# Optimization experiments

Hardware: AMD Instinct MI355X
Metric: run time of the kernel (lower is better)

The kernel has to match this reference:

```python
import jax, jax.numpy as jnp
import numpy as np

N_STATE = 1024
N_HEAD = 16
HEAD_DIM = N_STATE // N_HEAD
SEQLENS = [1024, 896, 768, 640, 512, 384, 896, 1024]  # sum = 6144
TOTAL = sum(SEQLENS)


def setup_inputs() -> dict:
    key = jax.random.key(0)
    ks = jax.random.split(key, 8)
    s = 0.02
    cu = jnp.asarray(np.concatenate([[0], np.cumsum(SEQLENS)]), dtype=jnp.int32)
    return {
        "x": jax.random.normal(ks[0], (TOTAL, N_STATE), jnp.float32),
        "cu_seqlens": cu,
        "Wq": jax.random.normal(ks[1], (N_STATE, N_STATE), jnp.float32) * s,
        "bq": jax.random.normal(ks[2], (N_STATE,), jnp.float32) * s,
        "Wk": jax.random.normal(ks[3], (N_STATE, N_STATE), jnp.float32) * s,
        "Wv": jax.random.normal(ks[4], (N_STATE, N_STATE), jnp.float32) * s,
        "bv": jax.random.normal(ks[5], (N_STATE,), jnp.float32) * s,
        "Wo": jax.random.normal(ks[6], (N_STATE, N_STATE), jnp.float32) * s,
        "bo": jax.random.normal(ks[7], (N_STATE,), jnp.float32) * s,
    }


def reference(x, cu_seqlens, Wq, bq, Wk, Wv, bv, Wo, bo):
    # cu_seqlens is a static (host) quantity in the original (used via .tolist())
    cu = np.asarray(jax.device_get(cu_seqlens))
    seqlens = cu[1:] - cu[:-1]
    B = len(seqlens)
    Lmax = int(seqlens.max())

    q = x @ Wq.T + bq              # [T, n_state]
    k = x @ Wk.T                   # key has no bias
    v = x @ Wv.T + bv

    # static pad/unpad index maps (honoring the ragged structure)
    ar = np.arange(Lmax)
    valid = ar[None, :] < seqlens[:, None]             # [B, Lmax]
    idx = np.where(valid, cu[:-1, None] + ar[None, :], 0)
    unpad_idx = np.nonzero(valid.reshape(-1))[0]       # flat positions of real tokens
    valid_j = jnp.asarray(valid)

    def pad(t):  # [T, n_state] -> [B, Lmax, H, D], zeros in padding
        p = jnp.where(valid_j[:, :, None], t[idx], 0.0)
        return p.reshape(B, Lmax, N_HEAD, HEAD_DIM)

    qp, kp, vp = pad(q), pad(k), pad(v)
    scale = HEAD_DIM ** -0.5
    # torch adds the bool mask (True->1.0) after masked_fill(mask==0, -max):
    # valid keys get +1.0 (softmax-invariant shift), invalid keys get -finfo.max
    big_neg = jnp.finfo(x.dtype).max
    add_mask = jnp.where(valid_j, 1.0, -big_neg)[:, None, None, :]  # [B,1,1,Lmax]

    scores = jnp.einsum("bqhd,bkhd->bhqk", qp, kp) * scale + add_mask
    weights = jax.nn.softmax(scores, axis=-1)
    ctx = jnp.einsum("bhqk,bkhd->bqhd", weights, vp)   # [B, Lmax, H, D]
    ctx_flat = ctx.reshape(B * Lmax, N_STATE)[unpad_idx]  # [T, n_state]
    return ctx_flat @ Wo.T + bo
```

## Files before the change

### kernel.cpp

```cpp
#include <hip/hip_runtime.h>

typedef unsigned short u16;
typedef unsigned int u32;
typedef __attribute__((ext_vector_type(8))) short bf16x8;
typedef __attribute__((ext_vector_type(4))) float f32x4;

#define MFMA_BF16(a, b, c) __builtin_amdgcn_mfma_f32_16x16x32_bf16((a), (b), (c), 0, 0, 0)

#define QSCALE 0.18033688011112042f

__device__ __forceinline__ u16 f2bf(float f) {
    union { float f; unsigned u; } v; v.f = f;
    return (u16)((v.u + 0x7FFFu + ((v.u >> 16) & 1u)) >> 16);
}

__device__ __forceinline__ u32 pkbf(float a, float b) {
    union { float f; unsigned u; } x, y; x.f = a; y.f = b;
    return ((x.u + 0x8000u) >> 16) | ((y.u + 0x8000u) & 0xFFFF0000u);
}

__device__ __forceinline__ void async16(const void* g, void* l) {
    __builtin_amdgcn_global_load_lds(
        (const __attribute__((address_space(1))) void*)g,
        (__attribute__((address_space(3))) void*)l, 16, 0, 0);
}

__global__ __launch_bounds__(256) void cvt_all(
    const float* __restrict__ x, const float* __restrict__ Wq, const float* __restrict__ Wk,
    const float* __restrict__ Wv, const float* __restrict__ Wo,
    u16* __restrict__ xb, u16* __restrict__ Wqb, u16* __restrict__ Wkb,
    u16* __restrict__ Wvb, u16* __restrict__ Wob) {
    int b = blockIdx.x;
    const float* src; u16* dst; int base;
    if (b < 6144)      { src = x;  dst = xb;  base = b; }
    else if (b < 7168) { src = Wq; dst = Wqb; base = b - 6144; }
    else if (b < 8192) { src = Wk; dst = Wkb; base = b - 7168; }
    else if (b < 9216) { src = Wv; dst = Wvb; base = b - 8192; }
    else               { src = Wo; dst = Wob; base = b - 9216; }
    int i = base * 256 + threadIdx.x;
    float4 v = ((const float4*)src)[i];
    unsigned long long pk = (unsigned long long)f2bf(v.x)
                          | ((unsigned long long)f2bf(v.y) << 16)
                          | ((unsigned long long)f2bf(v.z) << 32)
                          | ((unsigned long long)f2bf(v.w) << 48);
    *(unsigned long long*)(dst + (size_t)i * 4) = pk;
}

__global__ __launch_bounds__(256) void gemm_qkv(
    const u16* __restrict__ xb,
    const u16* __restrict__ Wqb, const u16* __restrict__ Wkb, const u16* __restrict__ Wvb,
    const float* __restrict__ bq, const float* __restrict__ bv,
    u16* __restrict__ qb, u16* __restrict__ kb, u16* __restrict__ vbT) {
    __shared__ __align__(16) u16 As[128 * 64];
    __shared__ __align__(16) u16 Bs[128 * 64];
    const int tid = threadIdx.x;
    const int m0 = blockIdx.x << 7;
    const int by = blockIdx.y;
    const int buf = by >> 3;
    const int n0 = (by & 7) << 7;
    const u16* __restrict__ W = (buf == 0) ? Wqb : (buf == 1) ? Wkb : Wvb;

    const int rr = tid >> 3;
    const int cg = tid & 7;
    const int wv = tid >> 6, lane = tid & 63, g = lane >> 4, c = lane & 15;
    const int wm = (wv & 1) << 6, wn = (wv >> 1) << 6;

    const int sw = (cg ^ (rr & 7)) << 3;
    const u16* gA[4]; const u16* gB[4];
#pragma unroll
    for (int r = 0; r < 4; ++r) {
        gA[r] = xb + (size_t)(m0 + (r << 5) + rr) * 1024 + sw;
        gB[r] = W + (size_t)(n0 + (r << 5) + rr) * 1024 + sw;
    }

    f32x4 zero = {0.f, 0.f, 0.f, 0.f};
    f32x4 acc[4][4];
#pragma unroll
    for (int i = 0; i < 4; ++i)
#pragma unroll
        for (int j = 0; j < 4; ++j) acc[i][j] = zero;

    if (buf < 2) {
        for (int kt = 0; kt < 16; ++kt) {
            const int k0 = kt << 6;
            __syncthreads();
#pragma unroll
            for (int r = 0; r < 4; ++r) {
                async16(gA[r] + k0, &As[(r << 11) + tid * 8]);
                async16(gB[r] + k0, &Bs[(r << 11) + tid * 8]);
            }
            __syncthreads();
#pragma unroll
            for (int ks = 0; ks < 2; ++ks) {
                bf16x8 af[4], bb[4];
#pragma unroll
                for (int i = 0; i < 4; ++i) {
                    int ra = wm + (i << 4) + c;
                    af[i] = *(const bf16x8*)(&As[ra * 64 + ((((ks << 2) + g) ^ (ra & 7)) << 3)]);
                    int rb = wn + (i << 4) + c;
                    bb[i] = *(const bf16x8*)(&Bs[rb * 64 + ((((ks << 2) + g) ^ (rb & 7)) << 3)]);
                }
#pragma unroll
                for (int i = 0; i < 4; ++i)
#pragma unroll
                    for (int j = 0; j < 4; ++j) acc[i][j] = MFMA_BF16(bb[j], af[i], acc[i][j]);
            }
        }
    } else {
        for (int kt = 0; kt < 16; ++kt) {
            const int k0 = kt << 6;
            __syncthreads();
#pragma unroll
            for (int r = 0; r < 4; ++r) {
                async16(gA[r] + k0, &As[(r << 11) + tid * 8]);
                async16(gB[r] + k0, &Bs[(r << 11) + tid * 8]);
            }
            __syncthreads();
#pragma unroll
            for (int ks = 0; ks < 2; ++ks) {
                bf16x8 af[4], bb[4];
#pragma unroll
                for (int i = 0; i < 4; ++i) {
                    int ra = wm + (i << 4) + c;
                    af[i] = *(const bf16x8*)(&As[ra * 64 + ((((ks << 2) + g) ^ (ra & 7)) << 3)]);
                    int rb = wn + (i << 4) + c;
                    bb[i] = *(const bf16x8*)(&Bs[rb * 64 + ((((ks << 2) + g) ^ (rb & 7)) << 3)]);
                }
#pragma unroll
                for (int i = 0; i < 4; ++i)
#pragma unroll
                    for (int j = 0; j < 4; ++j) acc[i][j] = MFMA_BF16(af[i], bb[j], acc[i][j]);
            }
        }
    }

    if (buf == 0) {
#pragma unroll
        for (int j = 0; j < 4; ++j) {
            int ncol = n0 + wn + (j << 4) + (g << 2);
            const float4 b4 = *(const float4*)(bq + ncol);
#pragma unroll
            for (int i = 0; i < 4; ++i) {
                const size_t mrow = (size_t)(m0 + wm + (i << 4) + c) * 1024;
                unsigned long long pk =
                      (unsigned long long)f2bf((acc[i][j][0] + b4.x) * QSCALE)
                    | ((unsigned long long)f2bf((acc[i][j][1] + b4.y) * QSCALE) << 16)
                    | ((unsigned long long)f2bf((acc[i][j][2] + b4.z) * QSCALE) << 32)
                    | ((unsigned long long)f2bf((acc[i][j][3] + b4.w) * QSCALE) << 48);
                *(unsigned long long*)(qb + mrow + ncol) = pk;
            }
        }
    } else if (buf == 1) {
#pragma unroll
        for (int j = 0; j < 4; ++j) {
            int ncol = n0 + wn + (j << 4) + (g << 2);
#pragma unroll
            for (int i = 0; i < 4; ++i) {
                const size_t mrow = (size_t)(m0 + wm + (i << 4) + c) * 1024;
                unsigned long long pk =
                      (unsigned long long)f2bf(acc[i][j][0])
                    | ((unsigned long long)f2bf(acc[i][j][1]) << 16)
                    | ((unsigned long long)f2bf(acc[i][j][2]) << 32)
                    | ((unsigned long long)f2bf(acc[i][j][3]) << 48);
                *(unsigned long long*)(kb + mrow + ncol) = pk;
            }
        }
    } else {
#pragma unroll
        for (int j = 0; j < 4; ++j) {
            int col = n0 + wn + (j << 4) + c;
            float bias = bv[col];
#pragma unroll
            for (int i = 0; i < 4; ++i) {
                int trow = m0 + wm + (i << 4) + (g << 2);
                unsigned long long pk =
                      (unsigned long long)f2bf(acc[i][j][0] + bias)
                    | ((unsigned long long)f2bf(acc[i][j][1] + bias) << 16)
                    | ((unsigned long long)f2bf(acc[i][j][2] + bias) << 32)
                    | ((unsigned long long)f2bf(acc[i][j][3] + bias) << 48);
                *(unsigned long long*)(vbT + (size_t)col * 6144 + trow) = pk;
            }
        }
    }
}

__global__ __launch_bounds__(256) void gemm_out(
    const u16* __restrict__ ctxb, const u16* __restrict__ Wob,
    const float* __restrict__ bo, float* __restrict__ out) {
    __shared__ __align__(16) u16 As[64 * 64];
    __shared__ __align__(16) u16 Bs[64 * 64];
    const int tid = threadIdx.x;
    const int m0 = blockIdx.x << 6;
    const int n0 = blockIdx.y << 6;
    const int rr = tid >> 3, cg = tid & 7;
    const int wv = tid >> 6, lane = tid & 63, g = lane >> 4, c = lane & 15;
    const int wm = (wv & 1) << 5, wn = (wv >> 1) << 5;

    const int sw = (cg ^ (rr & 7)) << 3;
    const u16* gA[2]; const u16* gB[2];
#pragma unroll
    for (int r = 0; r < 2; ++r) {
        gA[r] = ctxb + (size_t)(m0 + (r << 5) + rr) * 1024 + sw;
        gB[r] = Wob + (size_t)(n0 + (r << 5) + rr) * 1024 + sw;
    }

    f32x4 zero = {0.f, 0.f, 0.f, 0.f};
    f32x4 acc[2][2];
#pragma unroll
    for (int i = 0; i < 2; ++i)
#pragma unroll
        for (int j = 0; j < 2; ++j) acc[i][j] = zero;

    for (int kt = 0; kt < 16; ++kt) {
        const int k0 = kt << 6;
        __syncthreads();
#pragma unroll
        for (int r = 0; r < 2; ++r) {
            async16(gA[r] + k0, &As[(r << 11) + tid * 8]);
            async16(gB[r] + k0, &Bs[(r << 11) + tid * 8]);
        }
        __syncthreads();
#pragma unroll
        for (int ks = 0; ks < 2; ++ks) {
            bf16x8 af[2], bb[2];
#pragma unroll
            for (int i = 0; i < 2; ++i) {
                int ra = wm + (i << 4) + c;
                af[i] = *(const bf16x8*)(&As[ra * 64 + ((((ks << 2) + g) ^ (ra & 7)) << 3)]);
                int rb = wn + (i << 4) + c;
                bb[i] = *(const bf16x8*)(&Bs[rb * 64 + ((((ks << 2) + g) ^ (rb & 7)) << 3)]);
            }
#pragma unroll
            for (int i = 0; i < 2; ++i)
#pragma unroll
                for (int j = 0; j < 2; ++j) acc[i][j] = MFMA_BF16(bb[j], af[i], acc[i][j]);
        }
    }

#pragma unroll
    for (int i = 0; i < 2; ++i) {
        const size_t mrow = (size_t)(m0 + wm + (i << 4) + c) * 1024;
#pragma unroll
        for (int j = 0; j < 2; ++j) {
            int ncol = n0 + wn + (j << 4) + (g << 2);
            const float4 b4 = *(const float4*)(bo + ncol);
            float4 o;
            o.x = acc[i][j][0] + b4.x;
            o.y = acc[i][j][1] + b4.y;
            o.z = acc[i][j][2] + b4.z;
            o.w = acc[i][j][3] + b4.w;
            *(float4*)(out + mrow + ncol) = o;
        }
    }
}

__global__ __launch_bounds__(256) void attn_kernel(const u16* __restrict__ qb,
                                                   const u16* __restrict__ kb,
                                                   const u16* __restrict__ vbT,
                                                   u16* __restrict__ ctxb) {
    __shared__ __align__(16) u16 Ks[128 * 64];
    __shared__ __align__(16) u16 Vs[64 * 128];
    __shared__ __align__(16) u16 Ps[4 * 2048];

    const int tid = threadIdx.x;
    const int fid = blockIdx.x;
    const int xcd = fid & 7;
    const int slot = fid >> 3;
    const int h = (xcd << 1) + (slot >= 96 ? 1 : 0);
    const int q0 = (slot % 96) << 6;

    const int cuv[9] = {0, 1024, 1920, 2688, 3328, 3840, 4224, 5120, 6144};
    int s0 = 0, e0 = 6144;
#pragma unroll
    for (int i = 1; i < 8; ++i) {
        if (q0 >= cuv[i]) s0 = cuv[i];
        if (q0 < cuv[i] && cuv[i] < e0) e0 = cuv[i];
    }
    const int ntiles = (e0 - s0) >> 7;

    const int wv = tid >> 6, lane = tid & 63, g = lane >> 4, c = lane & 15;
    const int wrow = wv << 4;

    {
        const int rr = tid >> 3, cg = tid & 7;
#pragma unroll
        for (int r = 0; r < 2; ++r) {
            int row = (r << 5) + rr;
            async16(qb + (size_t)(q0 + row) * 1024 + (h << 6) + ((cg ^ (row & 7)) << 3),
                    Ps + (r << 11) + tid * 8);
        }
    }
    __syncthreads();

    bf16x8 qf[2];
#pragma unroll
    for (int ks = 0; ks < 2; ++ks) {
        int row = wrow + c;
        qf[ks] = *(const bf16x8*)(Ps + row * 64 + ((((ks << 2) + g) ^ (row & 7)) << 3));
    }

    float m_run = -1e30f, l_run = 0.f;
    f32x4 zero = {0.f, 0.f, 0.f, 0.f};
    f32x4 oacc[4];
#pragma unroll
    for (int nt = 0; nt < 4; ++nt) oacc[nt] = zero;

    const int pbase = (wv << 11) + c * 128;
    const int c7 = c & 7;

    for (int kt = 0; kt < ntiles; ++kt) {
        const int kv0 = s0 + (kt << 7);
        __syncthreads();
        {
            const int rr = tid >> 3, cg = tid & 7;
#pragma unroll
            for (int r = 0; r < 4; ++r) {
                int row = (r << 5) + rr;
                async16(kb + (size_t)(kv0 + row) * 1024 + (h << 6) + ((cg ^ (row & 7)) << 3),
                        Ks + (r << 11) + tid * 8);
            }
            const int rr2 = tid >> 4, cg2 = tid & 15;
#pragma unroll
            for (int r = 0; r < 4; ++r) {
                int row = (r << 4) + rr2;
                async16(vbT + (size_t)((h << 6) + row) * 6144 + kv0 + ((cg2 ^ (row & 15)) << 3),
                        Vs + (r << 11) + tid * 8);
            }
        }
        __syncthreads();

        f32x4 st[8];
#pragma unroll
        for (int mt = 0; mt < 8; ++mt) st[mt] = zero;
#pragma unroll
        for (int mt = 0; mt < 8; ++mt) {
            int row = (mt << 4) + c;
            int sw = row & 7;
#pragma unroll
            for (int ks = 0; ks < 2; ++ks) {
                bf16x8 kf = *(const bf16x8*)(&Ks[row * 64 + ((((ks << 2) + g) ^ sw) << 3)]);
                st[mt] = MFMA_BF16(kf, qf[ks], st[mt]);
            }
        }

        float mx = st[0][0];
#pragma unroll
        for (int mt = 0; mt < 8; ++mt)
#pragma unroll
            for (int r = 0; r < 4; ++r) mx = fmaxf(mx, st[mt][r]);
        mx = fmaxf(mx, __shfl_xor(mx, 16, 64));
        mx = fmaxf(mx, __shfl_xor(mx, 32, 64));
        float mnew = fmaxf(m_run, mx);
        float alpha = exp2f(m_run - mnew);
        m_run = mnew;

        float rsum = 0.f;
#pragma unroll
        for (int mt = 0; mt < 8; ++mt) {
            float p0 = exp2f(st[mt][0] - mnew);
            float p1 = exp2f(st[mt][1] - mnew);
            float p2 = exp2f(st[mt][2] - mnew);
            float p3 = exp2f(st[mt][3] - mnew);
            rsum += (p0 + p1) + (p2 + p3);
            int ph = ((mt << 2) + g) ^ (c7 << 1);
            *(uint2*)(Ps + pbase + (ph << 2)) = make_uint2(pkbf(p0, p1), pkbf(p2, p3));
        }
        rsum += __shfl_xor(rsum, 16, 64);
        rsum += __shfl_xor(rsum, 32, 64);
        l_run = l_run * alpha + rsum;

        float al[4];
#pragma unroll
        for (int r = 0; r < 4; ++r) al[r] = __shfl(alpha, (g << 2) + r, 16);
#pragma unroll
        for (int nt = 0; nt < 4; ++nt)
#pragma unroll
            for (int r = 0; r < 4; ++r) oacc[nt][r] *= al[r];

#pragma unroll
        for (int ks = 0; ks < 4; ++ks) {
            int pg = ((ks << 2) + g) ^ c7;
            bf16x8 pf = *(const bf16x8*)(Ps + pbase + (pg << 3));
#pragma unroll
            for (int nt = 0; nt < 4; ++nt) {
                int vrow = (nt << 4) + c;
                bf16x8 vf = *(const bf16x8*)(&Vs[vrow * 128 + ((((ks << 2) + g) ^ (vrow & 15)) << 3)]);
                oacc[nt] = MFMA_BF16(pf, vf, oacc[nt]);
            }
        }
    }

    float inv = 1.0f / l_run;
    float invr[4];
#pragma unroll
    for (int r = 0; r < 4; ++r) invr[r] = __shfl(inv, (g << 2) + r, 16);
#pragma unroll
    for (int r = 0; r < 4; ++r) {
        size_t rowoff = (size_t)(q0 + wrow + (g << 2) + r) * 1024 + (h << 6);
#pragma unroll
        for (int nt = 0; nt < 4; ++nt)
            ctxb[rowoff + (nt << 4) + c] = f2bf(oacc[nt][r] * invr[r]);
    }
}

extern "C" void kernel_launch(void* const* d_in, const int* in_sizes, int n_in,
                              void* d_out, int out_size, void* d_ws, size_t ws_size,
                              hipStream_t stream) {
    const float* x  = (const float*)d_in[0];
    const float* Wq = (const float*)d_in[2];
    const float* bq = (const float*)d_in[3];
    const float* Wk = (const float*)d_in[4];
    const float* Wv = (const float*)d_in[5];
    const float* bv = (const float*)d_in[6];
    const float* Wo = (const float*)d_in[7];
    const float* bo = (const float*)d_in[8];
    float* out = (float*)d_out;

    u16* ws = (u16*)d_ws;
    u16* xb   = ws;
    u16* Wqb  = xb + 6291456;
    u16* Wkb  = Wqb + 1048576;
    u16* Wvb  = Wkb + 1048576;
    u16* Wob  = Wvb + 1048576;
    u16* qb   = Wob + 1048576;
    u16* kb   = qb + 6291456;
    u16* vbT  = kb + 6291456;
    u16* ctxb = xb;

    cvt_all<<<10240, 256, 0, stream>>>(x, Wq, Wk, Wv, Wo, xb, Wqb, Wkb, Wvb, Wob);
    gemm_qkv<<<dim3(48, 24), 256, 0, stream>>>(xb, Wqb, Wkb, Wvb, bq, bv, qb, kb, vbT);
    attn_kernel<<<1536, 256, 0, stream>>>(qb, kb, vbT, ctxb);
    gemm_out<<<dim3(96, 16), 256, 0, stream>>>(ctxb, Wob, bo, out);
}
```

Measured before the change: 236.9 us.

## Process 128 query rows per attention block to reuse K/V tiles

Each attention block now handles 128 queries (two 16-row sub-tiles per wave) instead of 64, halving the grid to 768 blocks so every K/V tile loaded into LDS is reused across twice as many queries. The first K/V tile is prefetched together with Q before the loop, which removes one barrier pair per block. The XCD-aware head/query mapping is dropped in favour of a plain h = fid/48 mapping. In exchange, register pressure goes up (two sets of output accumulators and running statistics), there are fewer blocks to spread across CUs, and L2 locality per XCD may change.

```diff
diff --git a/kernel.cpp b/kernel.cpp
--- a/kernel.cpp
+++ b/kernel.cpp
@@ -264,10 +264,8 @@
 
     const int tid = threadIdx.x;
     const int fid = blockIdx.x;
-    const int xcd = fid & 7;
-    const int slot = fid >> 3;
-    const int h = (xcd << 1) + (slot >= 96 ? 1 : 0);
-    const int q0 = (slot % 96) << 6;
+    const int h = fid / 48;
+    const int q0 = (fid % 48) << 7;
 
     const int cuv[9] = {0, 1024, 1920, 2688, 3328, 3840, 4224, 5120, 6144};
     int s0 = 0, e0 = 6144;
@@ -279,127 +277,147 @@
     const int ntiles = (e0 - s0) >> 7;
 
     const int wv = tid >> 6, lane = tid & 63, g = lane >> 4, c = lane & 15;
-    const int wrow = wv << 4;
+    const int rr = tid >> 3, cg = tid & 7;
+    const int rr2 = tid >> 4, cg2 = tid & 15;
 
     {
-        const int rr = tid >> 3, cg = tid & 7;
-#pragma unroll
-        for (int r = 0; r < 2; ++r) {
+#pragma unroll
+        for (int r = 0; r < 4; ++r) {
             int row = (r << 5) + rr;
             async16(qb + (size_t)(q0 + row) * 1024 + (h << 6) + ((cg ^ (row & 7)) << 3),
                     Ps + (r << 11) + tid * 8);
         }
+#pragma unroll
+        for (int r = 0; r < 4; ++r) {
+            int row = (r << 5) + rr;
+            async16(kb + (size_t)(s0 + row) * 1024 + (h << 6) + ((cg ^ (row & 7)) << 3),
+                    Ks + (r << 11) + tid * 8);
+        }
+#pragma unroll
+        for (int r = 0; r < 4; ++r) {
+            int row = (r << 4) + rr2;
+            async16(vbT + (size_t)((h << 6) + row) * 6144 + s0 + ((cg2 ^ (row & 15)) << 3),
+                    Vs + (r << 11) + tid * 8);
+        }
     }
     __syncthreads();
 
-    bf16x8 qf[2];
-#pragma unroll
-    for (int ks = 0; ks < 2; ++ks) {
-        int row = wrow + c;
-        qf[ks] = *(const bf16x8*)(Ps + row * 64 + ((((ks << 2) + g) ^ (row & 7)) << 3));
-    }
-
-    float m_run = -1e30f, l_run = 0.f;
+    bf16x8 qf[2][2];
+#pragma unroll
+    for (int qh = 0; qh < 2; ++qh)
+#pragma unroll
+        for (int ks = 0; ks < 2; ++ks) {
+            int row = (wv << 5) + (qh << 4) + c;
+            qf[qh][ks] = *(const bf16x8*)(Ps + row * 64 + ((((ks << 2) + g) ^ (row & 7)) << 3));
+        }
+
+    float m_run[2] = {-1e30f, -1e30f}, l_run[2] = {0.f, 0.f};
     f32x4 zero = {0.f, 0.f, 0.f, 0.f};
-    f32x4 oacc[4];
-#pragma unroll
-    for (int nt = 0; nt < 4; ++nt) oacc[nt] = zero;
+    f32x4 oacc[2][4];
+#pragma unroll
+    for (int qh = 0; qh < 2; ++qh)
+#pragma unroll
+        for (int nt = 0; nt < 4; ++nt) oacc[qh][nt] = zero;
 
     const int pbase = (wv << 11) + c * 128;
     const int c7 = c & 7;
 
     for (int kt = 0; kt < ntiles; ++kt) {
-        const int kv0 = s0 + (kt << 7);
-        __syncthreads();
-        {
-            const int rr = tid >> 3, cg = tid & 7;
+        if (kt > 0) {
+            const int kv0 = s0 + (kt << 7);
+            __syncthreads();
 #pragma unroll
             for (int r = 0; r < 4; ++r) {
                 int row = (r << 5) + rr;
                 async16(kb + (size_t)(kv0 + row) * 1024 + (h << 6) + ((cg ^ (row & 7)) << 3),
                         Ks + (r << 11) + tid * 8);
             }
-            const int rr2 = tid >> 4, cg2 = tid & 15;
 #pragma unroll
             for (int r = 0; r < 4; ++r) {
                 int row = (r << 4) + rr2;
                 async16(vbT + (size_t)((h << 6) + row) * 6144 + kv0 + ((cg2 ^ (row & 15)) << 3),
                         Vs + (r << 11) + tid * 8);
             }
-        }
-        __syncthreads();
-
-        f32x4 st[8];
-#pragma unroll
-        for (int mt = 0; mt < 8; ++mt) st[mt] = zero;
-#pragma unroll
-        for (int mt = 0; mt < 8; ++mt) {
-            int row = (mt << 4) + c;
-            int sw = row & 7;
-#pragma unroll
-            for (int ks = 0; ks < 2; ++ks) {
-                bf16x8 kf = *(const bf16x8*)(&Ks[row * 64 + ((((ks << 2) + g) ^ sw) << 3)]);
-                st[mt] = MFMA_BF16(kf, qf[ks], st[mt]);
-            }
-        }
-
-        float mx = st[0][0];
-#pragma unroll
-        for (int mt = 0; mt < 8; ++mt)
-#pragma unroll
-            for (int r = 0; r < 4; ++r) mx = fmaxf(mx, st[mt][r]);
-        mx = fmaxf(mx, __shfl_xor(mx, 16, 64));
-        mx = fmaxf(mx, __shfl_xor(mx, 32, 64));
-        float mnew = fmaxf(m_run, mx);
-        float alpha = exp2f(m_run - mnew);
-        m_run = mnew;
-
-        float rsum = 0.f;
-#pragma unroll
-        for (int mt = 0; mt < 8; ++mt) {
-            float p0 = exp2f(st[mt][0] - mnew);
-            float p1 = exp2f(st[mt][1] - mnew);
-            float p2 = exp2f(st[mt][2] - mnew);
-            float p3 = exp2f(st[mt][3] - mnew);
-            rsum += (p0 + p1) + (p2 + p3);
-            int ph = ((mt << 2) + g) ^ (c7 << 1);
-            *(uint2*)(Ps + pbase + (ph << 2)) = make_uint2(pkbf(p0, p1), pkbf(p2, p3));
-        }
-        rsum += __shfl_xor(rsum, 16, 64);
-        rsum += __shfl_xor(rsum, 32, 64);
-        l_run = l_run * alpha + rsum;
-
-        float al[4];
-#pragma unroll
-        for (int r = 0; r < 4; ++r) al[r] = __shfl(alpha, (g << 2) + r, 16);
-#pragma unroll
-        for (int nt = 0; nt < 4; ++nt)
-#pragma unroll
-            for (int r = 0; r < 4; ++r) oacc[nt][r] *= al[r];
-
-#pragma unroll
-        for (int ks = 0; ks < 4; ++ks) {
-            int pg = ((ks << 2) + g) ^ c7;
-            bf16x8 pf = *(const bf16x8*)(Ps + pbase + (pg << 3));
-#pragma unroll
-            for (int nt = 0; nt < 4; ++nt) {
-                int vrow = (nt << 4) + c;
-                bf16x8 vf = *(const bf16x8*)(&Vs[vrow * 128 + ((((ks << 2) + g) ^ (vrow & 15)) << 3)]);
-                oacc[nt] = MFMA_BF16(pf, vf, oacc[nt]);
-            }
-        }
-    }
-
-    float inv = 1.0f / l_run;
-    float invr[4];
-#pragma unroll
-    for (int r = 0; r < 4; ++r) invr[r] = __shfl(inv, (g << 2) + r, 16);
-#pragma unroll
-    for (int r = 0; r < 4; ++r) {
-        size_t rowoff = (size_t)(q0 + wrow + (g << 2) + r) * 1024 + (h << 6);
-#pragma unroll
-        for (int nt = 0; nt < 4; ++nt)
-            ctxb[rowoff + (nt << 4) + c] = f2bf(oacc[nt][r] * invr[r]);
+            __syncthreads();
+        }
+
+#pragma unroll
+        for (int qh = 0; qh < 2; ++qh) {
+            f32x4 st[8];
+#pragma unroll
+            for (int mt = 0; mt < 8; ++mt) st[mt] = zero;
+#pragma unroll
+            for (int mt = 0; mt < 8; ++mt) {
+                int row = (mt << 4) + c;
+                int sw = row & 7;
+#pragma unroll
+                for (int ks = 0; ks < 2; ++ks) {
+                    bf16x8 kf = *(const bf16x8*)(&Ks[row * 64 + ((((ks << 2) + g) ^ sw) << 3)]);
+                    st[mt] = MFMA_BF16(kf, qf[qh][ks], st[mt]);
+                }
+            }
+
+            float mx = st[0][0];
+#pragma unroll
+            for (int mt = 0; mt < 8; ++mt)
+#pragma unroll
+                for (int r = 0; r < 4; ++r) mx = fmaxf(mx, st[mt][r]);
+            mx = fmaxf(mx, __shfl_xor(mx, 16, 64));
+            mx = fmaxf(mx, __shfl_xor(mx, 32, 64));
+            float mnew = fmaxf(m_run[qh], mx);
+            float alpha = exp2f(m_run[qh] - mnew);
+            m_run[qh] = mnew;
+
+            float rsum = 0.f;
+#pragma unroll
+            for (int mt = 0; mt < 8; ++mt) {
+                float p0 = exp2f(st[mt][0] - mnew);
+                float p1 = exp2f(st[mt][1] - mnew);
+                float p2 = exp2f(st[mt][2] - mnew);
+                float p3 = exp2f(st[mt][3] - mnew);
+                rsum += (p0 + p1) + (p2 + p3);
+                int ph = ((mt << 2) + g) ^ (c7 << 1);
+                *(uint2*)(Ps + pbase + (ph << 2)) = make_uint2(pkbf(p0, p1), pkbf(p2, p3));
+            }
+            rsum += __shfl_xor(rsum, 16, 64);
+            rsum += __shfl_xor(rsum, 32, 64);
+            l_run[qh] = l_run[qh] * alpha + rsum;
+
+            float al[4];
+#pragma unroll
+            for (int r = 0; r < 4; ++r) al[r] = __shfl(alpha, (g << 2) + r, 16);
+#pragma unroll
+            for (int nt = 0; nt < 4; ++nt)
+#pragma unroll
+                for (int r = 0; r < 4; ++r) oacc[qh][nt][r] *= al[r];
+
+#pragma unroll
+            for (int ks = 0; ks < 4; ++ks) {
+                int pg = ((ks << 2) + g) ^ c7;
+                bf16x8 pf = *(const bf16x8*)(Ps + pbase + (pg << 3));
+#pragma unroll
+                for (int nt = 0; nt < 4; ++nt) {
+                    int vrow = (nt << 4) + c;
+                    bf16x8 vf = *(const bf16x8*)(&Vs[vrow * 128 + ((((ks << 2) + g) ^ (vrow & 15)) << 3)]);
+                    oacc[qh][nt] = MFMA_BF16(pf, vf, oacc[qh][nt]);
+                }
+            }
+        }
+    }
+
+#pragma unroll
+    for (int qh = 0; qh < 2; ++qh) {
+        float inv = 1.0f / l_run[qh];
+        float invr[4];
+#pragma unroll
+        for (int r = 0; r < 4; ++r) invr[r] = __shfl(inv, (g << 2) + r, 16);
+#pragma unroll
+        for (int r = 0; r < 4; ++r) {
+            size_t rowoff = (size_t)(q0 + (wv << 5) + (qh << 4) + (g << 2) + r) * 1024 + (h << 6);
+#pragma unroll
+            for (int nt = 0; nt < 4; ++nt)
+                ctxb[rowoff + (nt << 4) + c] = f2bf(oacc[qh][nt][r] * invr[r]);
+        }
     }
 }
 
@@ -429,6 +447,6 @@
 
     cvt_all<<<10240, 256, 0, stream>>>(x, Wq, Wk, Wv, Wo, xb, Wqb, Wkb, Wvb, Wob);
     gemm_qkv<<<dim3(48, 24), 256, 0, stream>>>(xb, Wqb, Wkb, Wvb, bq, bv, qb, kb, vbT);
-    attn_kernel<<<1536, 256, 0, stream>>>(qb, kb, vbT, ctxb);
+    attn_kernel<<<768, 256, 0, stream>>>(qb, kb, vbT, ctxb);
     gemm_out<<<dim3(96, 16), 256, 0, stream>>>(ctxb, Wob, bo, out);
 }
```

Result: slower. 256.5 us (+8.3%).
